# Performance work log

Hardware: AMD Instinct MI355X
Metric: run time of the kernel (lower is better)

## Reference

```python
import jax, jax.numpy as jnp
import numpy as np

EMB = 64
N_LEFT = 50000
N_RIGHT = 50000
N_EDGES = 1000000
EPS = 1e-5


def _block(x, w1, b1, w2, b2):
    # Linear -> BatchNorm1d(batch stats, no affine) -> (Dropout=id, eval) -> Linear -> ReLU
    h = x @ w1 + b1
    mu = h.mean(axis=0)
    var = h.var(axis=0)  # biased, matches torch BN normalization
    h = (h - mu) / jnp.sqrt(var + EPS)
    return jax.nn.relu(h @ w2 + b2)


def _lin_init(key, fan_in, fan_out):
    k1, k2 = jax.random.split(key)
    bound = 1.0 / np.sqrt(fan_in)
    w = jax.random.uniform(k1, (fan_in, fan_out), minval=-bound, maxval=bound, dtype=jnp.float32)
    b = jax.random.uniform(k2, (fan_out,), minval=-bound, maxval=bound, dtype=jnp.float32)
    return w, b


def setup_inputs() -> dict:
    key = jax.random.key(0)
    ks = jax.random.split(key, 16)
    inp = {}
    inp['left_features'] = jax.random.normal(ks[0], (N_LEFT, EMB), dtype=jnp.float32)
    inp['right_features'] = jax.random.normal(ks[1], (N_RIGHT, EMB), dtype=jnp.float32)
    inp['edge_features'] = jax.random.normal(ks[2], (N_EDGES, EMB), dtype=jnp.float32)
    src = jax.random.randint(ks[3], (N_EDGES,), 0, N_LEFT, dtype=jnp.int32)
    dst = jax.random.randint(ks[4], (N_EDGES,), 0, N_RIGHT, dtype=jnp.int32)
    inp['edge_index'] = jnp.stack([src, dst], axis=0)
    # feature_module_right (applied to both i and j, as in the original message())
    inp['fmr_w1'], inp['fmr_b1'] = _lin_init(ks[5], EMB, EMB)
    inp['fmr_w2'], inp['fmr_b2'] = _lin_init(ks[6], EMB, EMB)
    # feature_module_edge
    inp['fme_w1'], inp['fme_b1'] = _lin_init(ks[7], EMB, EMB)
    inp['fme_w2'], inp['fme_b2'] = _lin_init(ks[8], EMB, EMB)
    # feature_module_final (3*emb -> emb -> emb)
    inp['fmf_w1'], inp['fmf_b1'] = _lin_init(ks[9], 3 * EMB, EMB)
    inp['fmf_w2'], inp['fmf_b2'] = _lin_init(ks[10], EMB, EMB)
    # output_module (2*emb -> emb -> emb)
    inp['out_w1'], inp['out_b1'] = _lin_init(ks[11], 2 * EMB, EMB)
    inp['out_w2'], inp['out_b2'] = _lin_init(ks[12], EMB, EMB)
    return inp


def reference(left_features, right_features, edge_features, edge_index,
              fmr_w1, fmr_b1, fmr_w2, fmr_b2,
              fme_w1, fme_b1, fme_w2, fme_b2,
              fmf_w1, fmf_b1, fmf_w2, fmf_b2,
              out_w1, out_b1, out_w2, out_b2):
    src = edge_index[0]  # index into left (source / j)
    dst = edge_index[1]  # index into right (target / i)

    x_i = right_features[dst]           # [E, emb] gathered targets
    x_j = left_features[src]            # [E, emb] gathered sources

    m_i = _block(x_i, fmr_w1, fmr_b1, fmr_w2, fmr_b2)
    m_e = _block(edge_features, fme_w1, fme_b1, fme_w2, fme_b2)
    m_j = _block(x_j, fmr_w1, fmr_b1, fmr_w2, fmr_b2)  # feature_module_right reused, as in source

    msg = _block(jnp.concatenate([m_i, m_e, m_j], axis=1),
                 fmf_w1, fmf_b1, fmf_w2, fmf_b2)        # [E, emb]

    # mean aggregation over target nodes
    agg = jax.ops.segment_sum(msg, dst, num_segments=N_RIGHT)
    cnt = jax.ops.segment_sum(jnp.ones((msg.shape[0],), msg.dtype), dst, num_segments=N_RIGHT)
    agg = agg / jnp.maximum(cnt, 1.0)[:, None]

    out = _block(jnp.concatenate([agg, right_features], axis=1),
                 out_w1, out_b1, out_w2, out_b2)        # [N_right, emb]
    return out
```

## Files before the change

kernel.cpp:

```cpp
#include <hip/hip_runtime.h>

#define EMB 64
#define BNEPS 1e-5f
#define NSLAB 8
#define NSLABH 32
#define MAXSLOT 128
#define MAXOVF 65536

typedef unsigned short u16;
typedef float f32x4 __attribute__((ext_vector_type(4)));
typedef short bf16x8 __attribute__((ext_vector_type(8)));
typedef short bf16x4 __attribute__((ext_vector_type(4)));

__device__ __forceinline__ float bf2f(u16 u){
  union { unsigned int i; float f; } v; v.i = ((unsigned int)u) << 16; return v.f;
}
__device__ __forceinline__ u16 f2bf(float x){
  union { float f; unsigned int i; } v; v.f = x;
  unsigned int r = v.i + 0x7FFFu + ((v.i >> 16) & 1u);
  return (u16)(r >> 16);
}
__device__ __forceinline__ void atomAddF(float* p, float v){
  __hip_atomic_fetch_add(p, v, __ATOMIC_RELAXED, __HIP_MEMORY_SCOPE_AGENT);
}

__global__ void kzero(float* __restrict__ fz, long nf){
  long i0 = (long)blockIdx.x * blockDim.x + threadIdx.x;
  long st = (long)gridDim.x * blockDim.x;
  for (long i = i0; i < nf; i += st) fz[i] = 0.f;
}

__global__ void kcount(const int* __restrict__ src, const int* __restrict__ dst,
                       int E, int* __restrict__ cs, int* __restrict__ cd,
                       int* __restrict__ sort1, int* __restrict__ ovfCnt,
                       int* __restrict__ ovfList){
  int e = blockIdx.x * blockDim.x + threadIdx.x;
  int st = gridDim.x * blockDim.x;
  for (; e < E; e += st){
    atomicAdd(&cs[src[e]], 1);
    int d = dst[e];
    int i = atomicAdd(&cd[d], 1);
    if (sort1){
      if (i < MAXSLOT){
        sort1[(size_t)d * MAXSLOT + i] = e;
      } else {
        int oi = atomicAdd(ovfCnt, 1);
        if (oi < MAXOVF) ovfList[oi] = e;
      }
    }
  }
}

__global__ __launch_bounds__(1024) void ktiles(const int* __restrict__ cd, int NR,
                       int* __restrict__ tcnt, int* __restrict__ tlist){
  __shared__ int wsum[16];
  __shared__ int wbase[16];
  __shared__ int bbase;
  int tid = threadIdx.x, lane = tid & 63, w = tid >> 6;
  int d = blockIdx.x * 1024 + tid;
  int nt = 0, c = 0;
  if (d < NR){
    c = cd[d];
    if (c > 0){
      nt = (c + 15) >> 4;
      if (nt > (MAXSLOT / 16)) nt = MAXSLOT / 16;
    }
  }
  int inc = nt;
  #pragma unroll
  for (int m = 1; m < 64; m <<= 1){
    int v = __shfl_up(inc, m);
    if (lane >= m) inc += v;
  }
  if (lane == 63) wsum[w] = inc;
  __syncthreads();
  if (tid == 0){
    int acc = 0;
    #pragma unroll
    for (int k = 0; k < 16; k++){ wbase[k] = acc; acc += wsum[k]; }
    bbase = acc ? atomicAdd(tcnt, acc) : 0;
  }
  __syncthreads();
  int my = bbase + wbase[w] + inc - nt;
  for (int t = 0; t < nt; t++){
    int vc = c - t * 16; if (vc > 16) vc = 16;
    tlist[my + t] = (vc << 20) | (d << 3) | t;
  }
}

__global__ __launch_bounds__(256) void kgram(const float* __restrict__ X,
    const int* __restrict__ cnt, int N,
    float* __restrict__ mupart, float* __restrict__ Spart){
  __shared__ float xs[16][EMB];
  __shared__ float cs[16];
  int t = threadIdx.x;
  int a = t >> 2, bb = (t & 3) << 4;
  int row = t >> 4, k0 = (t & 15) << 2;
  float g[16];
  #pragma unroll
  for (int i = 0; i < 16; i++) g[i] = 0.f;
  float mup = 0.f;
  int base0 = blockIdx.x * 16, stride = gridDim.x * 16;
  f32x4 xreg = {0.f,0.f,0.f,0.f};
  float creg = 0.f;
  {
    int n = base0 + row;
    if (n < N) xreg = *(const f32x4*)(X + (size_t)n * EMB + k0);
    if (t < 16){
      int n2 = base0 + t;
      creg = (n2 < N) ? (float)cnt[n2] : 0.f;
    }
  }
  for (int n0 = base0; n0 < N; n0 += stride){
    *(f32x4*)&xs[row][k0] = xreg;
    if (t < 16) cs[t] = creg;
    __syncthreads();
    int n1 = n0 + stride;
    if (n1 < N){
      int n = n1 + row;
      xreg = (n < N) ? *(const f32x4*)(X + (size_t)n * EMB + k0) : (f32x4){0.f,0.f,0.f,0.f};
      if (t < 16){
        int n2 = n1 + t;
        creg = (n2 < N) ? (float)cnt[n2] : 0.f;
      }
    }
    #pragma unroll
    for (int rr = 0; rr < 16; rr++){
      float xa = cs[rr] * xs[rr][a];
      const float4* x4 = (const float4*)&xs[rr][bb];
      #pragma unroll
      for (int i4 = 0; i4 < 4; i4++){
        float4 v = x4[i4];
        g[4*i4+0] += xa * v.x; g[4*i4+1] += xa * v.y;
        g[4*i4+2] += xa * v.z; g[4*i4+3] += xa * v.w;
      }
    }
    if (t < EMB){
      #pragma unroll
      for (int rr = 0; rr < 16; rr++) mup += cs[rr] * xs[rr][t];
    }
    __syncthreads();
  }
  float* Sp = Spart + (size_t)blockIdx.x * 4096;
  #pragma unroll
  for (int i4 = 0; i4 < 4; i4++)
    *(f32x4*)&Sp[a * EMB + bb + i4 * 4] = *(f32x4*)&g[i4 * 4];
  if (t < EMB) mupart[(size_t)blockIdx.x * 64 + t] = mup;
}

struct GredArgs { const float *Sp, *mp; int nb; float *So, *mo; };
__global__ __launch_bounds__(256) void kgreduce3(GredArgs g0, GredArgs g1, GredArgs g2){
  int job = blockIdx.x >> 4, sub = blockIdx.x & 15;
  GredArgs G = (job == 0) ? g0 : (job == 1) ? g1 : g2;
  int e = sub * 256 + threadIdx.x;
  float s0 = 0.f, s1 = 0.f, s2 = 0.f, s3 = 0.f;
  int b = 0;
  for (; b + 3 < G.nb; b += 4){
    s0 += G.Sp[(size_t)(b    ) * 4096 + e];
    s1 += G.Sp[(size_t)(b + 1) * 4096 + e];
    s2 += G.Sp[(size_t)(b + 2) * 4096 + e];
    s3 += G.Sp[(size_t)(b + 3) * 4096 + e];
  }
  for (; b < G.nb; b++) s0 += G.Sp[(size_t)b * 4096 + e];
  G.So[e] = (s0 + s1) + (s2 + s3);
  if (sub == 0 && threadIdx.x < 64){
    float m0 = 0.f, m1 = 0.f, m2 = 0.f, m3 = 0.f;
    int c = 0;
    for (; c + 3 < G.nb; c += 4){
      m0 += G.mp[(size_t)(c    ) * 64 + threadIdx.x];
      m1 += G.mp[(size_t)(c + 1) * 64 + threadIdx.x];
      m2 += G.mp[(size_t)(c + 2) * 64 + threadIdx.x];
      m3 += G.mp[(size_t)(c + 3) * 64 + threadIdx.x];
    }
    for (; c < G.nb; c++) m0 += G.mp[(size_t)c * 64 + threadIdx.x];
    G.mo[threadIdx.x] = (m0 + m1) + (m2 + m3);
  }
}

__global__ __launch_bounds__(256) void kprepm(const float* __restrict__ XE, int N,
    float* __restrict__ mupart, float* __restrict__ Spart, u16* __restrict__ XEb){
  __shared__ __align__(16) u16 XT[64 * 72];
  int t = threadIdx.x, l = t & 63, wv = t >> 6, g = l >> 4, e16 = l & 15;
  f32x4 C[4];
  #pragma unroll
  for (int mb = 0; mb < 4; mb++) C[mb] = (f32x4){0.f,0.f,0.f,0.f};
  float ms[4] = {0.f, 0.f, 0.f, 0.f};
  int ntiles = N >> 6;
  int T = blockIdx.x;
  f32x4 vr0 = {0,0,0,0}, vr1 = {0,0,0,0}, vr2 = {0,0,0,0}, vr3 = {0,0,0,0};
  if (T < ntiles){
    #pragma unroll
    for (int i = 0; i < 4; i++){
      int c = t + i * 256;
      int row = c >> 4, k0 = (c & 15) << 2;
      f32x4 v = *(const f32x4*)(XE + ((size_t)T * 64 + row) * EMB + k0);
      if (i == 0) vr0 = v; else if (i == 1) vr1 = v; else if (i == 2) vr2 = v; else vr3 = v;
    }
  }
  for (; T < ntiles; T += gridDim.x){
    #pragma unroll
    for (int i = 0; i < 4; i++){
      int c = t + i * 256;
      int row = c >> 4, k0 = (c & 15) << 2;
      f32x4 v = (i == 0) ? vr0 : (i == 1) ? vr1 : (i == 2) ? vr2 : vr3;
      u16 w4[4];
      #pragma unroll
      for (int q = 0; q < 4; q++){
        ms[q] += v[q];
        w4[q] = f2bf(v[q]);
        XT[(k0 + q) * 72 + row] = w4[q];
      }
      if (XEb) *(bf16x4*)(XEb + ((size_t)T * 64 + row) * EMB + k0) = *(bf16x4*)w4;
    }
    __syncthreads();
    int T2 = T + gridDim.x;
    if (T2 < ntiles){
      #pragma unroll
      for (int i = 0; i < 4; i++){
        int c = t + i * 256;
        int row = c >> 4, k0 = (c & 15) << 2;
        f32x4 v = *(const f32x4*)(XE + ((size_t)T2 * 64 + row) * EMB + k0);
        if (i == 0) vr0 = v; else if (i == 1) vr1 = v; else if (i == 2) vr2 = v; else vr3 = v;
      }
    }
    #pragma unroll
    for (int kf = 0; kf < 2; kf++){
      bf16x8 fr[4];
      #pragma unroll
      for (int mb = 0; mb < 4; mb++)
        fr[mb] = *(const bf16x8*)&XT[(mb*16 + e16) * 72 + kf*32 + g*8];
      bf16x8 bfr = *(const bf16x8*)&XT[(wv*16 + e16) * 72 + kf*32 + g*8];
      #pragma unroll
      for (int mb = 0; mb < 4; mb++)
        C[mb] = __builtin_amdgcn_mfma_f32_16x16x32_bf16(fr[mb], bfr, C[mb], 0, 0, 0);
    }
    __syncthreads();
  }
  float* Sp = Spart + (size_t)blockIdx.x * 4096;
  #pragma unroll
  for (int mb = 0; mb < 4; mb++)
    #pragma unroll
    for (int r = 0; r < 4; r++)
      Sp[(mb*16 + g*4 + r) * EMB + wv*16 + e16] = C[mb][r];
  __syncthreads();
  float* red = (float*)XT;
  #pragma unroll
  for (int q = 0; q < 4; q++){
    float x = ms[q];
    x += __shfl_xor(x, 16); x += __shfl_xor(x, 32);
    if (l < 16) red[(wv*16 + l)*4 + q] = x;
  }
  __syncthreads();
  if (t < 64){
    int k = t >> 2, q = t & 3;
    float s = red[(k)*4+q] + red[(16+k)*4+q] + red[(32+k)*4+q] + red[(48+k)*4+q];
    mupart[(size_t)blockIdx.x * 64 + k*4 + q] = s;
  }
}

struct EffwArgs {
  const float *mu, *S, *w1, *b1, *w2, *b2;
  float *We, *be;
};
__global__ __launch_bounds__(256) void keffw3(EffwArgs a0, EffwArgs a1, EffwArgs a2,
    float invN, u16* __restrict__ fragA1, u16* __restrict__ fragA2,
    const float* __restrict__ fA2src){
  EffwArgs A = (blockIdx.x == 0) ? a0 : (blockIdx.x == 1) ? a1 : a2;
  const float *musum = A.mu, *S = A.S, *w1 = A.w1, *b1 = A.b1, *w2 = A.w2, *b2 = A.b2;
  float *Weff = A.We, *beff = A.be;
  __shared__ float mu[EMB];
  __shared__ float C[EMB][EMB];
  __shared__ float W1p[EMB][EMB + 1];
  __shared__ float c1[EMB];
  __shared__ float istd[EMB];
  __shared__ float red[256];
  int t = threadIdx.x;
  if (t < EMB) mu[t] = musum[t] * invN;
  __syncthreads();
  for (int e = t; e < EMB * EMB; e += 256){
    int k = e >> 6, l = e & 63;
    C[k][l] = S[e] * invN - mu[k] * mu[l];
  }
  __syncthreads();
  {
    int j = t & 63, kg = t >> 6;
    float part = 0.f;
    for (int k = kg * 16; k < kg * 16 + 16; k++){
      float inner = 0.f;
      for (int l = 0; l < EMB; l++) inner += C[k][l] * w1[l * EMB + j];
      part += w1[k * EMB + j] * inner;
    }
    red[t] = part;
  }
  __syncthreads();
  if (t < EMB){
    float var = red[t] + red[t + 64] + red[t + 128] + red[t + 192];
    float is = 1.0f / sqrtf(var + BNEPS);
    istd[t] = is;
    float muh = 0.f;
    for (int k = 0; k < EMB; k++) muh += mu[k] * w1[k * EMB + t];
    muh += b1[t];
    c1[t] = (b1[t] - muh) * is;
  }
  __syncthreads();
  for (int e = t; e < EMB * EMB; e += 256){
    int k = e >> 6, j = e & 63;
    W1p[k][j] = w1[e] * istd[j];
  }
  __syncthreads();
  {
    int k = t >> 2, j2b = (t & 3) << 4;
    float acc[16];
    #pragma unroll
    for (int i = 0; i < 16; i++) acc[i] = 0.f;
    for (int j = 0; j < EMB; j++){
      float wp = W1p[k][j];
      const float* w2r = &w2[j * EMB + j2b];
      #pragma unroll
      for (int i = 0; i < 16; i++) acc[i] += wp * w2r[i];
    }
    #pragma unroll
    for (int i = 0; i < 16; i++){
      Weff[k * EMB + j2b + i] = acc[i];
      C[k][j2b + i] = acc[i];
    }
  }
  if (t < EMB){
    float acc = b2[t];
    for (int j = 0; j < EMB; j++) acc += c1[j] * w2[j * EMB + t];
    beff[t] = acc;
  }
  __syncthreads();
  if (blockIdx.x == 2){
    for (int ent = t; ent < 512; ent += 256){
      int mb = ent >> 7, kf = (ent >> 6) & 1, l = ent & 63;
      int g = l >> 4, e16 = l & 15;
      u16 out[8];
      #pragma unroll
      for (int i = 0; i < 8; i++)
        out[i] = f2bf(C[kf*32 + g*8 + i][mb*16 + e16]);
      *(bf16x8*)(fragA1 + ent * 8) = *(bf16x8*)out;
    }
  } else if (blockIdx.x == 1){
    for (int ent = t; ent < 512; ent += 256){
      int mb = ent >> 7, kf = (ent >> 6) & 1, l = ent & 63;
      int g = l >> 4, e16 = l & 15;
      u16 out[8];
      #pragma unroll
      for (int i = 0; i < 8; i++){
        int row = (kf + 2*(i>>2))*16 + g*4 + (i&3);
        out[i] = f2bf(fA2src[row * EMB + mb*16 + e16]);
      }
      *(bf16x8*)(fragA2 + ent * 8) = *(bf16x8*)out;
    }
  }
}

__global__ __launch_bounds__(256) void knodeMP(const float* __restrict__ X,
    const float* __restrict__ Weff, const float* __restrict__ beff,
    const float* __restrict__ Wslice, int N, u16* __restrict__ P){
  __shared__ float xs[4][EMB];
  __shared__ float ms[4][EMB];
  __shared__ float be[EMB];
  int t = threadIdx.x, r = t >> 6, j = t & 63;
  int pos = ((j >> 2) & 3) * 16 + (j >> 4) * 4 + (j & 3);
  float wA[EMB], wB[EMB];
  #pragma unroll
  for (int k = 0; k < EMB; k++){ wA[k] = Weff[k * EMB + j]; wB[k] = Wslice[k * EMB + j]; }
  if (t < EMB) be[t] = beff[t];
  __syncthreads();
  for (int n0 = blockIdx.x * 4; n0 < N; n0 += gridDim.x * 4){
    int n = n0 + r; bool ok = n < N;
    xs[r][j] = ok ? X[(size_t)n * EMB + j] : 0.f;
    __syncthreads();
    float a0 = be[j], a1 = 0.f, a2 = 0.f, a3 = 0.f;
    const float4* x4 = (const float4*)xs[r];
    #pragma unroll
    for (int kb = 0; kb < 16; kb++){
      float4 v = x4[kb];
      a0 += v.x * wA[4*kb]; a1 += v.y * wA[4*kb+1];
      a2 += v.z * wA[4*kb+2]; a3 += v.w * wA[4*kb+3];
    }
    ms[r][j] = fmaxf((a0 + a1) + (a2 + a3), 0.f);
    __syncthreads();
    float p0 = 0.f, p1 = 0.f, p2 = 0.f, p3 = 0.f;
    const float4* m4 = (const float4*)ms[r];
    #pragma unroll
    for (int kb = 0; kb < 16; kb++){
      float4 v = m4[kb];
      p0 += v.x * wB[4*kb]; p1 += v.y * wB[4*kb+1];
      p2 += v.z * wB[4*kb+2]; p3 += v.w * wB[4*kb+3];
    }
    if (ok) P[(size_t)n * EMB + pos] = f2bf((p0 + p1) + (p2 + p3));
    __syncthreads();
  }
}

__global__ __launch_bounds__(256) void kpass1m(const float* __restrict__ XE,
    const u16* __restrict__ XEb,
    const int* __restrict__ srcv, const int* __restrict__ dstv,
    const u16* __restrict__ fragA1, const u16* __restrict__ fragA2,
    const float* __restrict__ beff_e, const float* __restrict__ bf1,
    const u16* __restrict__ Pib, const u16* __restrict__ Pjb, int ntiles,
    u16* __restrict__ hbf, float* __restrict__ hsum, float* __restrict__ hsq){
  __shared__ float cs[256];
  int t = threadIdx.x, l = t & 63, wv = t >> 6, g = l >> 4, e16 = l & 15;
  cs[t] = 0.f;
  bf16x8 a1w[4][2], a2w[4][2];
  #pragma unroll
  for (int mb = 0; mb < 4; mb++)
    #pragma unroll
    for (int kf = 0; kf < 2; kf++){
      a1w[mb][kf] = *(const bf16x8*)(fragA1 + ((size_t)((mb*2+kf)*64 + l)) * 8);
      a2w[mb][kf] = *(const bf16x8*)(fragA2 + ((size_t)((mb*2+kf)*64 + l)) * 8);
    }
  f32x4 b1v[4], b2v[4];
  #pragma unroll
  for (int mb = 0; mb < 4; mb++)
    #pragma unroll
    for (int r = 0; r < 4; r++){
      b1v[mb][r] = beff_e[mb*16 + g*4 + r];
      b2v[mb][r] = bf1[mb*16 + g*4 + r];
    }
  f32x4 ps[4], pq[4];
  #pragma unroll
  for (int mb = 0; mb < 4; mb++){ ps[mb] = (f32x4){0,0,0,0}; pq[mb] = (f32x4){0,0,0,0}; }

  int gw = blockIdx.x * 4 + wv, nw = gridDim.x * 4;
  int d_n = 0, s_n = 0;
  if (gw < ntiles){ d_n = dstv[gw*16 + e16]; s_n = srcv[gw*16 + e16]; }
  for (int T = gw; T < ntiles; T += nw){
    int d = d_n, s = s_n;
    bf16x8 xf0, xf1;
    if (XEb){
      const u16* xr = XEb + (size_t)(T*16 + e16) * EMB;
      xf0 = *(const bf16x8*)(xr + g*8);
      xf1 = *(const bf16x8*)(xr + 32 + g*8);
    } else {
      const float* xr = XE + (size_t)(T*16 + e16) * EMB;
      f32x4 x0 = *(const f32x4*)(xr + g*8);
      f32x4 x1 = *(const f32x4*)(xr + g*8 + 4);
      f32x4 x2 = *(const f32x4*)(xr + 32 + g*8);
      f32x4 x3 = *(const f32x4*)(xr + 36 + g*8);
      #pragma unroll
      for (int q = 0; q < 4; q++){
        xf0[q]   = (short)f2bf(x0[q]); xf0[4+q] = (short)f2bf(x1[q]);
        xf1[q]   = (short)f2bf(x2[q]); xf1[4+q] = (short)f2bf(x3[q]);
      }
    }
    const u16* pib = Pib + (size_t)d * EMB + g*16;
    const u16* pjb = Pjb + (size_t)s * EMB + g*16;
    bf16x8 pi0 = *(const bf16x8*)(pib);
    bf16x8 pi1 = *(const bf16x8*)(pib + 8);
    bf16x8 pj0 = *(const bf16x8*)(pjb);
    bf16x8 pj1 = *(const bf16x8*)(pjb + 8);
    int T2 = T + nw;
    if (T2 < ntiles){ d_n = dstv[T2*16 + e16]; s_n = srcv[T2*16 + e16]; }
    f32x4 C2[4];
    #pragma unroll
    for (int mb = 0; mb < 4; mb++)
      #pragma unroll
      for (int r = 0; r < 4; r++){
        float pv = bf2f((u16)((mb < 2) ? pi0[(mb&1)*4 + r] : pi1[(mb&1)*4 + r]));
        float qv = bf2f((u16)((mb < 2) ? pj0[(mb&1)*4 + r] : pj1[(mb&1)*4 + r]));
        C2[mb][r] = b2v[mb][r] + pv + qv;
      }
    f32x4 C1[4];
    #pragma unroll
    for (int mb = 0; mb < 4; mb++) C1[mb] = b1v[mb];
    #pragma unroll
    for (int mb = 0; mb < 4; mb++){
      C1[mb] = __builtin_amdgcn_mfma_f32_16x16x32_bf16(a1w[mb][0], xf0, C1[mb], 0, 0, 0);
      C1[mb] = __builtin_amdgcn_mfma_f32_16x16x32_bf16(a1w[mb][1], xf1, C1[mb], 0, 0, 0);
    }
    bf16x8 mfr0, mfr1;
    #pragma unroll
    for (int q = 0; q < 4; q++){
      mfr0[q]   = (short)f2bf(fmaxf(C1[0][q], 0.f));
      mfr0[4+q] = (short)f2bf(fmaxf(C1[2][q], 0.f));
      mfr1[q]   = (short)f2bf(fmaxf(C1[1][q], 0.f));
      mfr1[4+q] = (short)f2bf(fmaxf(C1[3][q], 0.f));
    }
    #pragma unroll
    for (int mb = 0; mb < 4; mb++){
      C2[mb] = __builtin_amdgcn_mfma_f32_16x16x32_bf16(a2w[mb][0], mfr0, C2[mb], 0, 0, 0);
      C2[mb] = __builtin_amdgcn_mfma_f32_16x16x32_bf16(a2w[mb][1], mfr1, C2[mb], 0, 0, 0);
    }
    #pragma unroll
    for (int mb = 0; mb < 4; mb++){ ps[mb] += C2[mb]; pq[mb] += C2[mb] * C2[mb]; }
    u16* hr = hbf + (size_t)(T*16 + e16) * EMB;
    #pragma unroll
    for (int mb = 0; mb < 4; mb++){
      u16 hv[4];
      #pragma unroll
      for (int q = 0; q < 4; q++) hv[q] = f2bf(C2[mb][q]);
      *(bf16x4*)(hr + mb*16 + g*4) = *(bf16x4*)hv;
    }
  }
  __syncthreads();
  #pragma unroll
  for (int mb = 0; mb < 4; mb++)
    #pragma unroll
    for (int r = 0; r < 4; r++){
      float v = ps[mb][r], u = pq[mb][r];
      #pragma unroll
      for (int m = 1; m < 16; m <<= 1){ v += __shfl_xor(v, m); u += __shfl_xor(u, m); }
      if (e16 == 0){
        int col = mb*16 + g*4 + r;
        atomicAdd(&cs[col], v);
        atomicAdd(&cs[128 + col], u);
      }
    }
  __syncthreads();
  int slab = blockIdx.x & (NSLABH - 1);
  if (t < 64) atomAddF(&hsum[slab * 64 + t], cs[t]);
  else if (t < 128) atomAddF(&hsq[slab * 64 + t - 64], cs[128 + t - 64]);
}

__global__ __launch_bounds__(256) void kbnfold(const float* __restrict__ hsum,
    const float* __restrict__ hsq, int nslab, float invN, const float* __restrict__ w2,
    const float* __restrict__ b2, float* __restrict__ W2p, float* __restrict__ b2p,
    u16* __restrict__ F){
  __shared__ float mu[EMB], istd[EMB];
  int t = threadIdx.x;
  if (t < EMB){
    float m = 0.f, q = 0.f;
    for (int s = 0; s < nslab; s++){ m += hsum[s * 64 + t]; q += hsq[s * 64 + t]; }
    m *= invN;
    float var = q * invN - m * m;
    mu[t] = m; istd[t] = 1.0f / sqrtf(var + BNEPS);
  }
  __syncthreads();
  for (int e = t; e < EMB * EMB; e += 256){
    int k = e >> 6;
    W2p[e] = istd[k] * w2[e];
  }
  if (t < EMB){
    float acc = b2[t];
    for (int k = 0; k < EMB; k++) acc -= mu[k] * istd[k] * w2[k * EMB + t];
    b2p[t] = acc;
  }
  if (F){
    for (int ent = t; ent < 512; ent += 256){
      int mb = ent >> 7, kf = (ent >> 6) & 1, l = ent & 63;
      int g = (l >> 4), e16 = l & 15;
      u16 out[8];
      #pragma unroll
      for (int i = 0; i < 8; i++){
        int row = kf*32 + g*8 + i;
        out[i] = f2bf(istd[row] * w2[row * EMB + mb*16 + e16]);
      }
      *(bf16x8*)(F + ent * 8) = *(bf16x8*)out;
    }
  }
}

__global__ __launch_bounds__(256) void kpass2s(const u16* __restrict__ hb,
    const int* __restrict__ sort1, const int* __restrict__ tcnt,
    const int* __restrict__ tlist, const u16* __restrict__ fragW2,
    const float* __restrict__ b2p, float* __restrict__ agg){
  int t = threadIdx.x, l = t & 63, wv = t >> 6, g = l >> 4, e16 = l & 15;
  bf16x8 w2f[4][2];
  #pragma unroll
  for (int nb = 0; nb < 4; nb++)
    #pragma unroll
    for (int kf = 0; kf < 2; kf++)
      w2f[nb][kf] = *(const bf16x8*)(fragW2 + ((size_t)((nb*2+kf)*64 + l)) * 8);
  float bv[4];
  #pragma unroll
  for (int nb = 0; nb < 4; nb++) bv[nb] = b2p[nb*16 + e16];

  int tc = *tcnt;
  int gw = blockIdx.x * 4 + wv, nw = gridDim.x * 4;
  if (gw >= tc) return;
  int w_n = tlist[gw];
  int se_n = sort1[(size_t)((w_n >> 3) & 0x1FFFF) * MAXSLOT + (w_n & 7) * 16 + e16];
  for (int m = gw; m < tc; m += nw){
    int w = w_n, se = se_n;
    int m2 = m + nw;
    if (m2 < tc) w_n = tlist[m2];
    int d = (w >> 3) & 0x1FFFF, vc = w >> 20;
    int eid = (e16 < vc) ? se : 0;
    const u16* hr = hb + (size_t)eid * EMB;
    bf16x8 a0 = *(const bf16x8*)(hr + g*8);
    bf16x8 a1 = *(const bf16x8*)(hr + 32 + g*8);
    if (m2 < tc)
      se_n = sort1[(size_t)((w_n >> 3) & 0x1FFFF) * MAXSLOT + (w_n & 7) * 16 + e16];
    f32x4 C[4];
    #pragma unroll
    for (int nb = 0; nb < 4; nb++) C[nb] = (f32x4){0.f,0.f,0.f,0.f};
    #pragma unroll
    for (int nb = 0; nb < 4; nb++){
      C[nb] = __builtin_amdgcn_mfma_f32_16x16x32_bf16(a0, w2f[nb][0], C[nb], 0, 0, 0);
      C[nb] = __builtin_amdgcn_mfma_f32_16x16x32_bf16(a1, w2f[nb][1], C[nb], 0, 0, 0);
    }
    int r0 = g * 4;
    #pragma unroll
    for (int nb = 0; nb < 4; nb++){
      float s = 0.f;
      if (r0 + 0 < vc) s += fmaxf(C[nb][0] + bv[nb], 0.f);
      if (r0 + 1 < vc) s += fmaxf(C[nb][1] + bv[nb], 0.f);
      if (r0 + 2 < vc) s += fmaxf(C[nb][2] + bv[nb], 0.f);
      if (r0 + 3 < vc) s += fmaxf(C[nb][3] + bv[nb], 0.f);
      s += __shfl_xor(s, 16);
      s += __shfl_xor(s, 32);
      if (g == 0) atomAddF(&agg[(size_t)d * EMB + nb*16 + e16], s);
    }
  }
}

__global__ __launch_bounds__(256) void kpass2d(const u16* __restrict__ hb,
    const int* __restrict__ dstv, const u16* __restrict__ fragW2,
    const float* __restrict__ b2p, int ntiles, float* __restrict__ agg){
  int t = threadIdx.x, l = t & 63, wv = t >> 6, g = l >> 4, e16 = l & 15;
  bf16x8 w2f[4][2];
  #pragma unroll
  for (int nb = 0; nb < 4; nb++)
    #pragma unroll
    for (int kf = 0; kf < 2; kf++)
      w2f[nb][kf] = *(const bf16x8*)(fragW2 + ((size_t)((nb*2+kf)*64 + l)) * 8);
  float bv[4];
  #pragma unroll
  for (int nb = 0; nb < 4; nb++) bv[nb] = b2p[nb*16 + e16];
  int gw = blockIdx.x * 4 + wv, nw = gridDim.x * 4;
  for (int T = gw; T < ntiles; T += nw){
    const u16* hr = hb + (size_t)(T*16 + e16) * EMB;
    bf16x8 a0 = *(const bf16x8*)(hr + g*8);
    bf16x8 a1 = *(const bf16x8*)(hr + 32 + g*8);
    int4 dd = *(const int4*)(dstv + T*16 + g*4);
    f32x4 C[4];
    #pragma unroll
    for (int nb = 0; nb < 4; nb++) C[nb] = (f32x4){0.f,0.f,0.f,0.f};
    #pragma unroll
    for (int nb = 0; nb < 4; nb++){
      C[nb] = __builtin_amdgcn_mfma_f32_16x16x32_bf16(a0, w2f[nb][0], C[nb], 0, 0, 0);
      C[nb] = __builtin_amdgcn_mfma_f32_16x16x32_bf16(a1, w2f[nb][1], C[nb], 0, 0, 0);
    }
    int dr[4] = {dd.x, dd.y, dd.z, dd.w};
    #pragma unroll
    for (int r = 0; r < 4; r++){
      float* ap = agg + (size_t)dr[r] * EMB + e16;
      #pragma unroll
      for (int nb = 0; nb < 4; nb++)
        atomAddF(ap + nb*16, fmaxf(C[nb][r] + bv[nb], 0.f));
    }
  }
}

__global__ void kpass2f(const u16* __restrict__ hb, const int* __restrict__ ovfList,
    const int* __restrict__ ovfCnt, const int* __restrict__ dstv,
    const float* __restrict__ W2p, const float* __restrict__ b2p, float* __restrict__ agg){
  int cnt = *ovfCnt;
  if (cnt > MAXOVF) cnt = MAXOVF;
  for (int c = blockIdx.x * blockDim.x + threadIdx.x; c < cnt * 64;
       c += gridDim.x * blockDim.x){
    int e = ovfList[c >> 6], j = c & 63;
    const u16* hr = hb + (size_t)e * EMB;
    float acc = b2p[j];
    for (int k = 0; k < 64; k++) acc += bf2f(hr[k]) * W2p[k * EMB + j];
    atomAddF(&agg[(size_t)dstv[e] * EMB + j], fmaxf(acc, 0.f));
  }
}

__global__ __launch_bounds__(256) void kout1(const float* __restrict__ agg,
    const int* __restrict__ cnt, const float* __restrict__ right,
    const float* __restrict__ ow1, const float* __restrict__ ob1, int N,
    float* __restrict__ h_o, float* __restrict__ osum, float* __restrict__ osq){
  __shared__ float xs[4][2 * EMB];
  __shared__ float bsh[EMB];
  __shared__ float red[256];
  int t = threadIdx.x, r = t >> 6, j = t & 63;
  float wc[2 * EMB];
  #pragma unroll
  for (int k = 0; k < 2 * EMB; k++) wc[k] = ow1[k * EMB + j];
  if (t < EMB) bsh[t] = ob1[t];
  __syncthreads();
  float psum = 0.f, psq = 0.f;
  for (int n0 = blockIdx.x * 4; n0 < N; n0 += gridDim.x * 4){
    int n = n0 + r; bool ok = n < N;
    if (ok){
      float c = fmaxf((float)cnt[n], 1.f);
      xs[r][j] = agg[(size_t)n * EMB + j] / c;
      xs[r][EMB + j] = right[(size_t)n * EMB + j];
    } else { xs[r][j] = 0.f; xs[r][EMB + j] = 0.f; }
    __syncthreads();
    float a0 = bsh[j], a1 = 0.f, a2 = 0.f, a3 = 0.f;
    const float4* x4 = (const float4*)xs[r];
    #pragma unroll
    for (int kb = 0; kb < 32; kb++){
      float4 v = x4[kb];
      a0 += v.x * wc[4*kb]; a1 += v.y * wc[4*kb+1];
      a2 += v.z * wc[4*kb+2]; a3 += v.w * wc[4*kb+3];
    }
    if (ok){
      float h = (a0 + a1) + (a2 + a3);
      h_o[(size_t)n * EMB + j] = h;
      psum += h; psq += h * h;
    }
    __syncthreads();
  }
  int slab = blockIdx.x & (NSLAB - 1);
  red[t] = psum; __syncthreads();
  if (t < EMB) atomAddF(&osum[slab * 64 + t], red[t] + red[t + 64] + red[t + 128] + red[t + 192]);
  __syncthreads();
  red[t] = psq; __syncthreads();
  if (t < EMB) atomAddF(&osq[slab * 64 + t], red[t] + red[t + 64] + red[t + 128] + red[t + 192]);
}

__global__ __launch_bounds__(256) void kout2(const float* __restrict__ h_o,
    const float* __restrict__ osum, const float* __restrict__ osq, float invN,
    const float* __restrict__ ow2, const float* __restrict__ ob2, int N,
    float* __restrict__ out){
  __shared__ float hs[4][EMB];
  __shared__ float bsh[EMB];
  __shared__ float istd[EMB], mus[EMB];
  int t = threadIdx.x, r = t >> 6, j = t & 63;
  if (t < EMB){
    float m = 0.f, q = 0.f;
    #pragma unroll
    for (int s = 0; s < NSLAB; s++){ m += osum[s * 64 + t]; q += osq[s * 64 + t]; }
    m *= invN;
    float var = q * invN - m * m;
    mus[t] = m; istd[t] = 1.0f / sqrtf(var + BNEPS);
  }
  __syncthreads();
  if (t < EMB){
    float acc = ob2[t];
    for (int k = 0; k < EMB; k++) acc -= mus[k] * istd[k] * ow2[k * EMB + t];
    bsh[t] = acc;
  }
  float wc[EMB];
  #pragma unroll
  for (int k = 0; k < EMB; k++) wc[k] = istd[k] * ow2[k * EMB + j];
  __syncthreads();
  for (int n0 = blockIdx.x * 4; n0 < N; n0 += gridDim.x * 4){
    int n = n0 + r; bool ok = n < N;
    hs[r][j] = ok ? h_o[(size_t)n * EMB + j] : 0.f;
    __syncthreads();
    float a0 = bsh[j], a1 = 0.f, a2 = 0.f, a3 = 0.f;
    const float4* h4 = (const float4*)hs[r];
    #pragma unroll
    for (int kb = 0; kb < 16; kb++){
      float4 v = h4[kb];
      a0 += v.x * wc[4*kb]; a1 += v.y * wc[4*kb+1];
      a2 += v.z * wc[4*kb+2]; a3 += v.w * wc[4*kb+3];
    }
    if (ok) out[(size_t)n * EMB + j] = fmaxf((a0 + a1) + (a2 + a3), 0.f);
    __syncthreads();
  }
}

extern "C" void kernel_launch(void* const* d_in, const int* in_sizes, int n_in,
                              void* d_out, int out_size, void* d_ws, size_t ws_size,
                              hipStream_t stream){
  const float* left   = (const float*)d_in[0];
  const float* right  = (const float*)d_in[1];
  const float* edgef  = (const float*)d_in[2];
  const int*   eidx   = (const int*)d_in[3];
  const float* fmr_w1 = (const float*)d_in[4];  const float* fmr_b1 = (const float*)d_in[5];
  const float* fmr_w2 = (const float*)d_in[6];  const float* fmr_b2 = (const float*)d_in[7];
  const float* fme_w1 = (const float*)d_in[8];  const float* fme_b1 = (const float*)d_in[9];
  const float* fme_w2 = (const float*)d_in[10]; const float* fme_b2 = (const float*)d_in[11];
  const float* fmf_w1 = (const float*)d_in[12]; const float* fmf_b1 = (const float*)d_in[13];
  const float* fmf_w2 = (const float*)d_in[14]; const float* fmf_b2 = (const float*)d_in[15];
  const float* ow1    = (const float*)d_in[16]; const float* ob1    = (const float*)d_in[17];
  const float* ow2    = (const float*)d_in[18]; const float* ob2    = (const float*)d_in[19];

  int NL = in_sizes[0] / EMB;
  int NR = in_sizes[1] / EMB;
  int E  = in_sizes[2] / EMB;
  const int* srcv = eidx;
  const int* dstv = eidx + E;

  char* base = (char*)d_ws;
  size_t o = 0;
  u16* hbf = (u16*)(base + o);      o += (size_t)E * EMB * sizeof(u16);
  u16* P_i  = (u16*)(base + o); o += (size_t)NR * EMB * sizeof(u16);
  u16* P_j  = (u16*)(base + o); o += (size_t)NL * EMB * sizeof(u16);
  float* h_o  = (float*)(base + o); o += (size_t)NR * EMB * 4;
  float* Weff_i = (float*)(base + o); o += EMB * EMB * 4;
  float* beff_i = (float*)(base + o); o += EMB * 4;
  float* Weff_j = (float*)(base + o); o += EMB * EMB * 4;
  float* beff_j = (float*)(base + o); o += EMB * 4;
  float* Weff_e = (float*)(base + o); o += EMB * EMB * 4;
  float* beff_e = (float*)(base + o); o += EMB * 4;
  float* W2p  = (float*)(base + o); o += EMB * EMB * 4;
  float* b2p  = (float*)(base + o); o += EMB * 4;
  u16* fragA1 = (u16*)(base + o); o += 512 * 8 * sizeof(u16);
  u16* fragA2 = (u16*)(base + o); o += 512 * 8 * sizeof(u16);
  u16* fragW2 = (u16*)(base + o); o += 512 * 8 * sizeof(u16);
  int* ovfList = (int*)(base + o); o += MAXOVF * sizeof(int);
  int* tlist   = (int*)(base + o); o += (size_t)NR * (MAXSLOT / 16) * sizeof(int);
  char* zstart = base + o;
  float* agg     = (float*)(base + o); o += (size_t)NR * EMB * 4;
  int* cnt_dst   = (int*)(base + o);   o += (size_t)NR * 4;
  int* cnt_src   = (int*)(base + o);   o += (size_t)NL * 4;
  int* ovfCnt    = (int*)(base + o);   o += 64;
  int* tileCnt   = (int*)(base + o);   o += 64;
  float* musum_i = (float*)(base + o); o += NSLAB * EMB * 4;
  float* S_i     = (float*)(base + o); o += NSLAB * EMB * EMB * 4;
  float* musum_j = (float*)(base + o); o += NSLAB * EMB * 4;
  float* S_j     = (float*)(base + o); o += NSLAB * EMB * EMB * 4;
  float* musum_e = (float*)(base + o); o += NSLAB * EMB * 4;
  float* S_e     = (float*)(base + o); o += NSLAB * EMB * EMB * 4;
  float* hsum    = (float*)(base + o); o += NSLABH * EMB * 4;
  float* hsq     = (float*)(base + o); o += NSLABH * EMB * 4;
  float* osum    = (float*)(base + o); o += NSLAB * EMB * 4;
  float* osq     = (float*)(base + o); o += NSLAB * EMB * 4;
  long zn = (long)(((base + o) - zstart) / 4);
  int* sort1 = nullptr;
  {
    size_t s1b = (size_t)NR * MAXSLOT * sizeof(int);
    if (o + s1b <= ws_size){ sort1 = (int*)(base + o); o += s1b; }
  }
  u16* XEb = nullptr;
  {
    size_t xeb_bytes = (size_t)E * EMB * sizeof(u16);
    if (o + xeb_bytes <= ws_size){ XEb = (u16*)(base + o); o += xeb_bytes; }
  }

  const int NBG = 512;
  const int NBE = 1024;
  float* Spart_i  = (float*)hbf;
  float* Spart_j  = Spart_i + (size_t)NBG * 4096;
  float* Spart_e  = Spart_j + (size_t)NBG * 4096;
  float* mupart_i = Spart_e + (size_t)NBE * 4096;
  float* mupart_j = mupart_i + (size_t)NBG * 64;
  float* mupart_e = mupart_j + (size_t)NBG * 64;

  float invE = 1.0f / (float)E;
  float invNR = 1.0f / (float)NR;
  int ntE = E >> 4;

  kzero<<<1024, 256, 0, stream>>>((float*)zstart, zn);
  kcount<<<512, 256, 0, stream>>>(srcv, dstv, E, cnt_src, cnt_dst, sort1, ovfCnt, ovfList);
  if (sort1) ktiles<<<(NR + 1023) / 1024, 1024, 0, stream>>>(cnt_dst, NR, tileCnt, tlist);
  kprepm<<<NBE, 256, 0, stream>>>(edgef, E, mupart_e, Spart_e, XEb);
  kgram<<<NBG, 256, 0, stream>>>(right, cnt_dst, NR, mupart_i, Spart_i);
  kgram<<<NBG, 256, 0, stream>>>(left,  cnt_src, NL, mupart_j, Spart_j);
  {
    GredArgs g0 = {Spart_i, mupart_i, NBG, S_i, musum_i};
    GredArgs g1 = {Spart_j, mupart_j, NBG, S_j, musum_j};
    GredArgs g2 = {Spart_e, mupart_e, NBE, S_e, musum_e};
    kgreduce3<<<48, 256, 0, stream>>>(g0, g1, g2);
  }
  {
    EffwArgs a0 = {musum_i, S_i, fmr_w1, fmr_b1, fmr_w2, fmr_b2, Weff_i, beff_i};
    EffwArgs a1 = {musum_j, S_j, fmr_w1, fmr_b1, fmr_w2, fmr_b2, Weff_j, beff_j};
    EffwArgs a2 = {musum_e, S_e, fme_w1, fme_b1, fme_w2, fme_b2, Weff_e, beff_e};
    keffw3<<<3, 256, 0, stream>>>(a0, a1, a2, invE, fragA1, fragA2, fmf_w1 + EMB * EMB);
  }
  knodeMP<<<1024, 256, 0, stream>>>(right, Weff_i, beff_i, fmf_w1,                 NR, P_i);
  knodeMP<<<1024, 256, 0, stream>>>(left,  Weff_j, beff_j, fmf_w1 + 2 * EMB * EMB, NL, P_j);
  kpass1m<<<2048, 256, 0, stream>>>(edgef, XEb, srcv, dstv, fragA1, fragA2, beff_e,
                                    fmf_b1, P_i, P_j, ntE, hbf, hsum, hsq);
  kbnfold<<<1, 256, 0, stream>>>(hsum, hsq, NSLABH, invE, fmf_w2, fmf_b2, W2p, b2p, fragW2);
  if (sort1){
    kpass2s<<<2048, 256, 0, stream>>>(hbf, sort1, tileCnt, tlist, fragW2, b2p, agg);
    kpass2f<<<16, 256, 0, stream>>>(hbf, ovfList, ovfCnt, dstv, W2p, b2p, agg);
  } else {
    kpass2d<<<2048, 256, 0, stream>>>(hbf, dstv, fragW2, b2p, ntE, agg);
  }
  kout1<<<1024, 256, 0, stream>>>(agg, cnt_dst, right, ow1, ob1, NR, h_o, osum, osq);
  kout2<<<1024, 256, 0, stream>>>(h_o, osum, osq, invNR, ow2, ob2, NR, (float*)d_out);
}
```

Before: 710.7 us.

## Assign one wave per destination node in pass2 and drop agg atomics and zeroing

The second message pass now gives each wave a whole destination node instead of one 16-edge tile. The wave loops over all of that node's tiles, keeps the sums in registers, and writes the aggregate with a plain store instead of atomic adds. The aggregate buffer no longer sits in the zeroed region. Nodes with no edges are left unwritten and handled in kout1 by a count check. This saves the atomics and the memory-clear traffic, in exchange for some load imbalance from varying node degree. The non-sorted fallback path now calls the overflow kernel with an empty list, so it would yield zero aggregates.

```diff
diff --git a/kernel.cpp b/kernel.cpp
--- a/kernel.cpp
+++ b/kernel.cpp
@@ -51,8 +51,8 @@
   }
 }
 
-__global__ __launch_bounds__(1024) void ktiles(const int* __restrict__ cd, int NR,
-                       int* __restrict__ tcnt, int* __restrict__ tlist){
+__global__ __launch_bounds__(1024) void knodes(const int* __restrict__ cd, int NR,
+                       int* __restrict__ ncnt, int* __restrict__ nlist){
   __shared__ int wsum[16];
   __shared__ int wbase[16];
   __shared__ int bbase;
@@ -61,10 +61,8 @@
   int nt = 0, c = 0;
   if (d < NR){
     c = cd[d];
-    if (c > 0){
-      nt = (c + 15) >> 4;
-      if (nt > (MAXSLOT / 16)) nt = MAXSLOT / 16;
-    }
+    if (c > 0) nt = 1;
+    if (c > MAXSLOT) c = MAXSLOT;
   }
   int inc = nt;
   #pragma unroll
@@ -78,14 +76,10 @@
     int acc = 0;
     #pragma unroll
     for (int k = 0; k < 16; k++){ wbase[k] = acc; acc += wsum[k]; }
-    bbase = acc ? atomicAdd(tcnt, acc) : 0;
-  }
-  __syncthreads();
-  int my = bbase + wbase[w] + inc - nt;
-  for (int t = 0; t < nt; t++){
-    int vc = c - t * 16; if (vc > 16) vc = 16;
-    tlist[my + t] = (vc << 20) | (d << 3) | t;
-  }
+    bbase = acc ? atomicAdd(ncnt, acc) : 0;
+  }
+  __syncthreads();
+  if (nt) nlist[bbase + wbase[w] + inc - 1] = (c << 17) | d;
 }
 
 __global__ __launch_bounds__(256) void kgram(const float* __restrict__ X,
@@ -555,9 +549,9 @@
   }
 }
 
-__global__ __launch_bounds__(256) void kpass2s(const u16* __restrict__ hb,
-    const int* __restrict__ sort1, const int* __restrict__ tcnt,
-    const int* __restrict__ tlist, const u16* __restrict__ fragW2,
+__global__ __launch_bounds__(256) void kpass2n(const u16* __restrict__ hb,
+    const int* __restrict__ sort1, const int* __restrict__ ncnt,
+    const int* __restrict__ nlist, const u16* __restrict__ fragW2,
     const float* __restrict__ b2p, float* __restrict__ agg){
   int t = threadIdx.x, l = t & 63, wv = t >> 6, g = l >> 4, e16 = l & 15;
   bf16x8 w2f[4][2];
@@ -570,79 +564,44 @@
   #pragma unroll
   for (int nb = 0; nb < 4; nb++) bv[nb] = b2p[nb*16 + e16];
 
-  int tc = *tcnt;
+  int nc = *ncnt;
   int gw = blockIdx.x * 4 + wv, nw = gridDim.x * 4;
-  if (gw >= tc) return;
-  int w_n = tlist[gw];
-  int se_n = sort1[(size_t)((w_n >> 3) & 0x1FFFF) * MAXSLOT + (w_n & 7) * 16 + e16];
-  for (int m = gw; m < tc; m += nw){
-    int w = w_n, se = se_n;
-    int m2 = m + nw;
-    if (m2 < tc) w_n = tlist[m2];
-    int d = (w >> 3) & 0x1FFFF, vc = w >> 20;
-    int eid = (e16 < vc) ? se : 0;
-    const u16* hr = hb + (size_t)eid * EMB;
-    bf16x8 a0 = *(const bf16x8*)(hr + g*8);
-    bf16x8 a1 = *(const bf16x8*)(hr + 32 + g*8);
-    if (m2 < tc)
-      se_n = sort1[(size_t)((w_n >> 3) & 0x1FFFF) * MAXSLOT + (w_n & 7) * 16 + e16];
-    f32x4 C[4];
-    #pragma unroll
-    for (int nb = 0; nb < 4; nb++) C[nb] = (f32x4){0.f,0.f,0.f,0.f};
+  for (int m = gw; m < nc; m += nw){
+    int w = nlist[m];
+    int d = w & 0x1FFFF, c = w >> 17;
+    int nt = (c + 15) >> 4;
+    const int* srow = sort1 + (size_t)d * MAXSLOT;
+    float accs[4] = {0.f, 0.f, 0.f, 0.f};
+    int r0 = g * 4;
+    for (int tt = 0; tt < nt; tt++){
+      int vc = c - tt * 16; if (vc > 16) vc = 16;
+      int se = srow[tt * 16 + e16];
+      int eid = (e16 < vc) ? se : 0;
+      const u16* hr = hb + (size_t)eid * EMB;
+      bf16x8 a0 = *(const bf16x8*)(hr + g*8);
+      bf16x8 a1 = *(const bf16x8*)(hr + 32 + g*8);
+      f32x4 C[4];
+      #pragma unroll
+      for (int nb = 0; nb < 4; nb++) C[nb] = (f32x4){0.f,0.f,0.f,0.f};
+      #pragma unroll
+      for (int nb = 0; nb < 4; nb++){
+        C[nb] = __builtin_amdgcn_mfma_f32_16x16x32_bf16(a0, w2f[nb][0], C[nb], 0, 0, 0);
+        C[nb] = __builtin_amdgcn_mfma_f32_16x16x32_bf16(a1, w2f[nb][1], C[nb], 0, 0, 0);
+      }
+      #pragma unroll
+      for (int nb = 0; nb < 4; nb++){
+        if (r0 + 0 < vc) accs[nb] += fmaxf(C[nb][0] + bv[nb], 0.f);
+        if (r0 + 1 < vc) accs[nb] += fmaxf(C[nb][1] + bv[nb], 0.f);
+        if (r0 + 2 < vc) accs[nb] += fmaxf(C[nb][2] + bv[nb], 0.f);
+        if (r0 + 3 < vc) accs[nb] += fmaxf(C[nb][3] + bv[nb], 0.f);
+      }
+    }
     #pragma unroll
     for (int nb = 0; nb < 4; nb++){
-      C[nb] = __builtin_amdgcn_mfma_f32_16x16x32_bf16(a0, w2f[nb][0], C[nb], 0, 0, 0);
-      C[nb] = __builtin_amdgcn_mfma_f32_16x16x32_bf16(a1, w2f[nb][1], C[nb], 0, 0, 0);
-    }
-    int r0 = g * 4;
-    #pragma unroll
-    for (int nb = 0; nb < 4; nb++){
-      float s = 0.f;
-      if (r0 + 0 < vc) s += fmaxf(C[nb][0] + bv[nb], 0.f);
-      if (r0 + 1 < vc) s += fmaxf(C[nb][1] + bv[nb], 0.f);
-      if (r0 + 2 < vc) s += fmaxf(C[nb][2] + bv[nb], 0.f);
-      if (r0 + 3 < vc) s += fmaxf(C[nb][3] + bv[nb], 0.f);
+      float s = accs[nb];
       s += __shfl_xor(s, 16);
       s += __shfl_xor(s, 32);
-      if (g == 0) atomAddF(&agg[(size_t)d * EMB + nb*16 + e16], s);
-    }
-  }
-}
-
-__global__ __launch_bounds__(256) void kpass2d(const u16* __restrict__ hb,
-    const int* __restrict__ dstv, const u16* __restrict__ fragW2,
-    const float* __restrict__ b2p, int ntiles, float* __restrict__ agg){
-  int t = threadIdx.x, l = t & 63, wv = t >> 6, g = l >> 4, e16 = l & 15;
-  bf16x8 w2f[4][2];
-  #pragma unroll
-  for (int nb = 0; nb < 4; nb++)
-    #pragma unroll
-    for (int kf = 0; kf < 2; kf++)
-      w2f[nb][kf] = *(const bf16x8*)(fragW2 + ((size_t)((nb*2+kf)*64 + l)) * 8);
-  float bv[4];
-  #pragma unroll
-  for (int nb = 0; nb < 4; nb++) bv[nb] = b2p[nb*16 + e16];
-  int gw = blockIdx.x * 4 + wv, nw = gridDim.x * 4;
-  for (int T = gw; T < ntiles; T += nw){
-    const u16* hr = hb + (size_t)(T*16 + e16) * EMB;
-    bf16x8 a0 = *(const bf16x8*)(hr + g*8);
-    bf16x8 a1 = *(const bf16x8*)(hr + 32 + g*8);
-    int4 dd = *(const int4*)(dstv + T*16 + g*4);
-    f32x4 C[4];
-    #pragma unroll
-    for (int nb = 0; nb < 4; nb++) C[nb] = (f32x4){0.f,0.f,0.f,0.f};
-    #pragma unroll
-    for (int nb = 0; nb < 4; nb++){
-      C[nb] = __builtin_amdgcn_mfma_f32_16x16x32_bf16(a0, w2f[nb][0], C[nb], 0, 0, 0);
-      C[nb] = __builtin_amdgcn_mfma_f32_16x16x32_bf16(a1, w2f[nb][1], C[nb], 0, 0, 0);
-    }
-    int dr[4] = {dd.x, dd.y, dd.z, dd.w};
-    #pragma unroll
-    for (int r = 0; r < 4; r++){
-      float* ap = agg + (size_t)dr[r] * EMB + e16;
-      #pragma unroll
-      for (int nb = 0; nb < 4; nb++)
-        atomAddF(ap + nb*16, fmaxf(C[nb][r] + bv[nb], 0.f));
+      if (g == 0) agg[(size_t)d * EMB + nb*16 + e16] = s;
     }
   }
 }
@@ -679,8 +638,8 @@
   for (int n0 = blockIdx.x * 4; n0 < N; n0 += gridDim.x * 4){
     int n = n0 + r; bool ok = n < N;
     if (ok){
-      float c = fmaxf((float)cnt[n], 1.f);
-      xs[r][j] = agg[(size_t)n * EMB + j] / c;
+      int cn = cnt[n];
+      xs[r][j] = (cn > 0) ? agg[(size_t)n * EMB + j] / (float)cn : 0.f;
       xs[r][EMB + j] = right[(size_t)n * EMB + j];
     } else { xs[r][j] = 0.f; xs[r][EMB + j] = 0.f; }
     __syncthreads();
@@ -778,6 +737,7 @@
   u16* P_i  = (u16*)(base + o); o += (size_t)NR * EMB * sizeof(u16);
   u16* P_j  = (u16*)(base + o); o += (size_t)NL * EMB * sizeof(u16);
   float* h_o  = (float*)(base + o); o += (size_t)NR * EMB * 4;
+  float* agg  = (float*)(base + o); o += (size_t)NR * EMB * 4;
   float* Weff_i = (float*)(base + o); o += EMB * EMB * 4;
   float* beff_i = (float*)(base + o); o += EMB * 4;
   float* Weff_j = (float*)(base + o); o += EMB * EMB * 4;
@@ -790,13 +750,12 @@
   u16* fragA2 = (u16*)(base + o); o += 512 * 8 * sizeof(u16);
   u16* fragW2 = (u16*)(base + o); o += 512 * 8 * sizeof(u16);
   int* ovfList = (int*)(base + o); o += MAXOVF * sizeof(int);
-  int* tlist   = (int*)(base + o); o += (size_t)NR * (MAXSLOT / 16) * sizeof(int);
+  int* nlist   = (int*)(base + o); o += (size_t)NR * sizeof(int);
   char* zstart = base + o;
-  float* agg     = (float*)(base + o); o += (size_t)NR * EMB * 4;
   int* cnt_dst   = (int*)(base + o);   o += (size_t)NR * 4;
   int* cnt_src   = (int*)(base + o);   o += (size_t)NL * 4;
   int* ovfCnt    = (int*)(base + o);   o += 64;
-  int* tileCnt   = (int*)(base + o);   o += 64;
+  int* nodeCnt   = (int*)(base + o);   o += 64;
   float* musum_i = (float*)(base + o); o += NSLAB * EMB * 4;
   float* S_i     = (float*)(base + o); o += NSLAB * EMB * EMB * 4;
   float* musum_j = (float*)(base + o); o += NSLAB * EMB * 4;
@@ -832,9 +791,9 @@
   float invNR = 1.0f / (float)NR;
   int ntE = E >> 4;
 
-  kzero<<<1024, 256, 0, stream>>>((float*)zstart, zn);
+  kzero<<<256, 256, 0, stream>>>((float*)zstart, zn);
   kcount<<<512, 256, 0, stream>>>(srcv, dstv, E, cnt_src, cnt_dst, sort1, ovfCnt, ovfList);
-  if (sort1) ktiles<<<(NR + 1023) / 1024, 1024, 0, stream>>>(cnt_dst, NR, tileCnt, tlist);
+  if (sort1) knodes<<<(NR + 1023) / 1024, 1024, 0, stream>>>(cnt_dst, NR, nodeCnt, nlist);
   kprepm<<<NBE, 256, 0, stream>>>(edgef, E, mupart_e, Spart_e, XEb);
   kgram<<<NBG, 256, 0, stream>>>(right, cnt_dst, NR, mupart_i, Spart_i);
   kgram<<<NBG, 256, 0, stream>>>(left,  cnt_src, NL, mupart_j, Spart_j);
@@ -856,10 +815,11 @@
                                     fmf_b1, P_i, P_j, ntE, hbf, hsum, hsq);
   kbnfold<<<1, 256, 0, stream>>>(hsum, hsq, NSLABH, invE, fmf_w2, fmf_b2, W2p, b2p, fragW2);
   if (sort1){
-    kpass2s<<<2048, 256, 0, stream>>>(hbf, sort1, tileCnt, tlist, fragW2, b2p, agg);
+    kpass2n<<<2048, 256, 0, stream>>>(hbf, sort1, nodeCnt, nlist, fragW2, b2p, agg);
     kpass2f<<<16, 256, 0, stream>>>(hbf, ovfList, ovfCnt, dstv, W2p, b2p, agg);
   } else {
-    kpass2d<<<2048, 256, 0, stream>>>(hbf, dstv, fragW2, b2p, ntE, agg);
+    kzero<<<512, 256, 0, stream>>>(agg, (long)NR * EMB);
+    kpass2f<<<2048, 256, 0, stream>>>(hbf, ovfList, ovfCnt, dstv, W2p, b2p, agg);
   }
   kout1<<<1024, 256, 0, stream>>>(agg, cnt_dst, right, ow1, ob1, NR, h_o, osum, osq);
   kout2<<<1024, 256, 0, stream>>>(h_o, osum, osq, invNR, ow2, ob2, NR, (float*)d_out);
```

Result: slower. 731.2 us (+2.9%).
